# Kernel tuning notes

Measured on AMD Instinct MI355X. Metric: run time of the kernel, lower is better.

## Reference

```python
import jax, jax.numpy as jnp
import numpy as np

H = 64      # h_dim
E = 64      # embedding_dim
L = 100     # latent_dim
T = 30      # seq_len
DT = 0.03

def _leaky(x):
    return jnp.where(x >= 0, x, 0.01 * x)  # nn.LeakyReLU default slope

def _mlp(h, Ws, bs, Wf, bf):
    # 3 stacked [H,H] LeakyReLU layers + final [L,H] layer, LeakyReLU after EVERY layer (as in source)
    for i in range(Ws.shape[0]):
        h = _leaky(h @ Ws[i].T + bs[i])
    return _leaky(h @ Wf.T + bf)

def _lstm_step(h, c, gates):
    # torch LSTM gate order: i, f, g, o
    i, f, g, o = jnp.split(gates, 4, axis=-1)
    c = jax.nn.sigmoid(f) * c + jax.nn.sigmoid(i) * jnp.tanh(g)
    h = jax.nn.sigmoid(o) * jnp.tanh(c)
    return h, c

def _forward(expert_traj, init_state, eps,
             W_se, b_se,
             W_ih_e, W_hh_e, b_ih_e, b_hh_e,
             mean_Ws, mean_bs, mean_Wf, mean_bf,
             lv_Ws, lv_bs, lv_Wf, lv_bf,
             W_init, b_init,
             W_ih_d, W_hh_d, b_ih_d, b_hh_d,
             W_c, b_c):
    B = expert_traj.shape[0]
    # --- encode: relative positions ---
    rel_xy = jnp.concatenate([expert_traj[:, :1, :2],
                              expert_traj[:, 1:, :2] - expert_traj[:, :-1, :2]], axis=1)
    inp = jnp.concatenate([rel_xy, expert_traj[:, :, 2:]], axis=-1)  # [B,T,4]
    emb = inp @ W_se.T + b_se                                        # [B,T,E]
    x_seq = jnp.swapaxes(emb, 0, 1)                                  # [T,B,E] seq-major
    # precompute input projection for all timesteps in one GEMM
    xp = x_seq @ W_ih_e.T + (b_ih_e + b_hh_e)                        # [T,B,4H]
    h0 = jnp.zeros((B, H), dtype=expert_traj.dtype)
    c0 = jnp.zeros((B, H), dtype=expert_traj.dtype)
    def enc_step(carry, xp_t):
        h, c = carry
        h, c = _lstm_step(h, c, xp_t + h @ W_hh_e.T)
        return (h, c), None
    (hT, _), _ = jax.lax.scan(enc_step, (h0, c0), xp)
    mu = _mlp(hT, mean_Ws, mean_bs, mean_Wf, mean_bf)                # [B,L]
    log_var = _mlp(hT, lv_Ws, lv_bs, lv_Wf, lv_bf)                   # [B,L]
    # --- reparameterize + tanh ---
    z = jnp.tanh(eps * jnp.exp(0.5 * log_var) + mu)
    # --- decode ---
    dh = z @ W_init.T + b_init                                       # [B,H], h0 = c0 = dh
    bias_d = b_ih_d + b_hh_d
    def dec_step(carry, _):
        h, c, prev = carry
        xe = prev @ W_se.T + b_se                                    # spatial embedding of state
        h, c = _lstm_step(h, c, xe @ W_ih_d.T + h @ W_hh_d.T + bias_d)
        ctrl = h @ W_c.T + b_c                                       # [B,2]
        pedal = ctrl[:, 0]
        steer = jnp.clip(ctrl[:, 1], -0.5, 0.5)
        x_t, y_t, psi, v = prev[:, 0], prev[:, 1], prev[:, 2], prev[:, 3]
        v1 = jnp.clip(v + pedal * DT, 0.0, 30.0)
        psi_dot = jnp.clip(v * jnp.tan(steer) / 2.5, -3.14 / 2, 3.14 / 2)
        cur = jnp.stack([x_t + v * jnp.cos(psi) * DT,
                         y_t + v * jnp.sin(psi) * DT,
                         psi + psi_dot * DT,
                         v1], axis=1)
        return (h, c, cur), cur
    _, traj = jax.lax.scan(dec_step, (dh, dh, init_state), None, length=T)
    recons = jnp.swapaxes(traj, 0, 1)                                # [B,T,4]
    return recons, expert_traj, mu, log_var

def setup_inputs() -> dict:
    key = jax.random.key(0)
    ks = jax.random.split(key, 32)
    B = 16384
    s = 0.05
    def p(k, shape):
        return jax.random.normal(k, shape, dtype=jnp.float32) * s
    return {
        "expert_traj": jax.random.normal(ks[0], (B, T, 4), dtype=jnp.float32),
        "init_state": jax.random.normal(ks[1], (B, 4), dtype=jnp.float32),
        "eps": jax.random.normal(ks[2], (B, L), dtype=jnp.float32),
        "W_se": p(ks[3], (E, 4)), "b_se": p(ks[4], (E,)),
        "W_ih_e": p(ks[5], (4 * H, E)), "W_hh_e": p(ks[6], (4 * H, H)),
        "b_ih_e": p(ks[7], (4 * H,)), "b_hh_e": p(ks[8], (4 * H,)),
        "mean_Ws": p(ks[9], (3, H, H)), "mean_bs": p(ks[10], (3, H)),
        "mean_Wf": p(ks[11], (L, H)), "mean_bf": p(ks[12], (L,)),
        "lv_Ws": p(ks[13], (3, H, H)), "lv_bs": p(ks[14], (3, H)),
        "lv_Wf": p(ks[15], (L, H)), "lv_bf": p(ks[16], (L,)),
        "W_init": p(ks[17], (H, L)), "b_init": p(ks[18], (H,)),
        "W_ih_d": p(ks[19], (4 * H, E)), "W_hh_d": p(ks[20], (4 * H, H)),
        "b_ih_d": p(ks[21], (4 * H,)), "b_hh_d": p(ks[22], (4 * H,)),
        "W_c": p(ks[23], (2, H)), "b_c": p(ks[24], (2,)),
    }

def reference(expert_traj, init_state, eps,
              W_se, b_se,
              W_ih_e, W_hh_e, b_ih_e, b_hh_e,
              mean_Ws, mean_bs, mean_Wf, mean_bf,
              lv_Ws, lv_bs, lv_Wf, lv_bf,
              W_init, b_init,
              W_ih_d, W_hh_d, b_ih_d, b_hh_d,
              W_c, b_c):
    return _forward(expert_traj, init_state, eps,
                    W_se, b_se,
                    W_ih_e, W_hh_e, b_ih_e, b_hh_e,
                    mean_Ws, mean_bs, mean_Wf, mean_bf,
                    lv_Ws, lv_bs, lv_Wf, lv_bf,
                    W_init, b_init,
                    W_ih_d, W_hh_d, b_ih_d, b_hh_d,
                    W_c, b_c)
```

## Files before the change

### kernel.cpp

```cpp
#include <hip/hip_runtime.h>

typedef unsigned short u16;
typedef unsigned int u32;
typedef __attribute__((ext_vector_type(8))) short bf16x8;
typedef __attribute__((ext_vector_type(4))) float f32x4;

#define B_TOT 16384
#define RR 16
#define BLK 256
#define NBLK (B_TOT / RR)
#define TT 30
#define LL 100
#define DTC 0.03f
#define L2E 1.44269504088896f

#define HST 104
#define HBUF (RR * HST)

#define OFF_H   0
#define OFF_XS  6656
#define OFF_INP 10752
#define OFF_ZB  14592
#define SMEM_SZ 18944

#define WS_WHHE  0
#define WS_WHHD  18432
#define WS_MWS   36864
#define WS_LWS   49152
#define WS_MWF   61440
#define WS_LWF   67840
#define WS_WINIT 74240
#define WS_TOTAL 82432

__device__ __forceinline__ float bf2f(u16 u) {
    union { u32 i; float f; } v; v.i = ((u32)u) << 16; return v.f;
}
__device__ __forceinline__ u16 f2bf(float f) {
    union { float f; u32 i; } v; v.f = f;
    return (u16)((v.i + 0x7FFFu + ((v.i >> 16) & 1u)) >> 16);
}
__device__ __forceinline__ u16 f2bf_t(float f) {
    union { float f; u32 i; } v; v.f = f;
    return (u16)(v.i >> 16);
}
__device__ __forceinline__ float rcpf(float x) { return __builtin_amdgcn_rcpf(x); }
__device__ __forceinline__ float ex2(float x) { return __builtin_amdgcn_exp2f(x); }
__device__ __forceinline__ float tanh_(float x) {
    x = fminf(fmaxf(x, -15.f), 15.f);
    float e = __expf(2.f * x);
    return (e - 1.f) * rcpf(e + 1.f);
}
__device__ __forceinline__ float leaky(float x) { return x >= 0.f ? x : 0.01f * x; }
__device__ __forceinline__ f32x4 mfma16(bf16x8 a, bf16x8 b, f32x4 c) {
    return __builtin_amdgcn_mfma_f32_16x16x32_bf16(a, b, c, 0, 0, 0);
}

__global__ void setup_kernel(
    const float* __restrict__ W_se, const float* __restrict__ b_se,
    const float* __restrict__ W_ih_e, const float* __restrict__ W_hh_e,
    const float* __restrict__ b_ih_e, const float* __restrict__ b_hh_e,
    const float* __restrict__ W_ih_d, const float* __restrict__ W_hh_d,
    const float* __restrict__ b_ih_d, const float* __restrict__ b_hh_d,
    const float* __restrict__ mean_Ws, const float* __restrict__ lv_Ws,
    const float* __restrict__ mean_Wf, const float* __restrict__ lv_Wf,
    const float* __restrict__ W_init, u16* __restrict__ ws)
{
    const int gid = blockIdx.x * 256 + threadIdx.x;
    const int nth = gridDim.x * 256;
    for (int i = gid; i < 512; i += nth) {
        int which = i >> 8, row = i & 255, g = row >> 6;
        float s = (g == 2) ? 2.f * L2E : L2E;
        const float* wih = (which ? W_ih_d : W_ih_e) + row * 64;
        float f0=0,f1=0,f2=0,f3=0,fb=0;
        for (int e = 0; e < 64; ++e) {
            float w = wih[e];
            f0 = fmaf(w, W_se[e*4+0], f0);
            f1 = fmaf(w, W_se[e*4+1], f1);
            f2 = fmaf(w, W_se[e*4+2], f2);
            f3 = fmaf(w, W_se[e*4+3], f3);
            fb = fmaf(w, b_se[e], fb);
        }
        fb += (which ? b_ih_d : b_ih_e)[row] + (which ? b_hh_d : b_hh_e)[row];
        u16* dst = ws + (which ? WS_WHHD : WS_WHHE) + row * 72 + 64;
        dst[0]=f2bf(f0*s); dst[1]=f2bf(f1*s); dst[2]=f2bf(f2*s); dst[3]=f2bf(f3*s);
        dst[4]=f2bf(fb*s); dst[5]=0; dst[6]=0; dst[7]=0;
    }
    for (int i = gid; i < 2*16384; i += nth) {
        int which = i >= 16384;
        int j = which ? i - 16384 : i;
        int row = j >> 6, k = j & 63, g = row >> 6;
        float s = (g == 2) ? 2.f * L2E : L2E;
        const float* whh = which ? W_hh_d : W_hh_e;
        ws[(which ? WS_WHHD : WS_WHHE) + row*72 + k] = f2bf(whh[j] * s);
    }
    for (int i = gid; i < 12288; i += nth) {
        ws[WS_MWS + i] = f2bf(mean_Ws[i]);
        ws[WS_LWS + i] = f2bf(lv_Ws[i]);
    }
    for (int i = gid; i < 6400; i += nth) {
        ws[WS_MWF + i] = f2bf(mean_Wf[i]);
        ws[WS_LWF + i] = f2bf(lv_Wf[i]);
    }
    for (int i = gid; i < 8192; i += nth) {
        int r = i >> 7, k = i & 127;
        ws[WS_WINIT + i] = (k < LL) ? f2bf(W_init[r*LL + k]) : (u16)0;
    }
}

__global__ __launch_bounds__(BLK, 4) void vae_lstm_kernel(
    const float* __restrict__ expert, const float* __restrict__ init_state,
    const float* __restrict__ eps, const u16* __restrict__ ws,
    const float* __restrict__ mean_bs, const float* __restrict__ mean_bf,
    const float* __restrict__ lv_bs, const float* __restrict__ lv_bf,
    const float* __restrict__ b_init, const float* __restrict__ W_c,
    const float* __restrict__ b_c,
    float* __restrict__ out_recons, float* __restrict__ out_expert,
    float* __restrict__ out_mu, float* __restrict__ out_lv)
{
    const int tid = threadIdx.x;
    const int wv = tid >> 6;
    const int l = tid & 63;
    const int lcol = l & 15;
    const int quad = l >> 4;
    const int ubase = wv * 16;
    const int b0 = blockIdx.x * RR;

    __shared__ __align__(16) char smem[SMEM_SZ];
    u16* Hb  = (u16*)(smem + OFF_H);
    u16* XS  = (u16*)(smem + OFF_XS);
    u16* XA  = XS;
    u16* XB  = XS + RR*64;
    u16* inp = (u16*)(smem + OFF_INP);
    u16* zB  = (u16*)(smem + OFF_ZB);
    float* sc = (float*)XS;

    {
        u32* hz = (u32*)Hb;
        for (int idx = tid; idx < 2*RR*52; idx += BLK) hz[idx] = 0;
        u32* zz = (u32*)zB;
        for (int idx = tid; idx < RR*68; idx += BLK) zz[idx] = 0;
        __syncthreads();
        if (tid < 32) Hb[(tid >> 4)*HBUF + (tid & 15)*HST + 68] = 0x3F80;
        const int base = b0 * (TT*4);
        for (int idx = tid; idx < RR*TT*4; idx += BLK) {
            int row = idx / 120, q = idx % 120;
            int t = q >> 2, k = q & 3;
            float v = expert[base + idx];
            out_expert[base + idx] = v;
            float r = v;
            if (k < 2 && t > 0) r = v - expert[base + idx - 4];
            u16 hv = f2bf(r);
            inp[row*120 + q] = hv;
            if (t == 0) Hb[row*HST + 64 + k] = hv;
        }
        __syncthreads();
    }

    float cst[4] = {};
    float hval[4];
    bf16x8 bw[4][3];

    auto build_bw = [&](const u16* wsW) {
#pragma unroll
        for (int g = 0; g < 4; ++g) {
            const u16* wr = wsW + (g*64 + ubase + lcol) * 72;
            bw[g][0] = *(const bf16x8*)(wr + quad*8);
            bw[g][1] = *(const bf16x8*)(wr + 32 + quad*8);
            bw[g][2] = *(const bf16x8*)(wr + 64);
        }
#pragma unroll
        for (int g = 0; g < 4; ++g)
#pragma unroll
            for (int kk = 0; kk < 3; ++kk)
                asm volatile("" : "+v"(bw[g][kk]));
    };

    auto lstm_step = [&](const u16* Hc, u16* Hn) {
        const u16* hrow = Hc + lcol*HST;
        bf16x8 a0 = *(const bf16x8*)(hrow + quad*8);
        bf16x8 a1 = *(const bf16x8*)(hrow + 32 + quad*8);
        bf16x8 a2 = *(const bf16x8*)(hrow + 64 + quad*8);
        f32x4 acc[4];
#pragma unroll
        for (int g = 0; g < 4; ++g) {
            f32x4 z = {0.f, 0.f, 0.f, 0.f};
            z = mfma16(a0, bw[g][0], z);
            z = mfma16(a1, bw[g][1], z);
            acc[g] = mfma16(a2, bw[g][2], z);
        }
#pragma unroll
        for (int r = 0; r < 4; ++r) {
            float Ei = ex2(-acc[0][r]);
            float Ef = ex2(-acc[1][r]);
            float Eg = ex2(-acc[2][r]);
            float Eo = ex2(-acc[3][r]);
            float P = (1.f + Ei) * (1.f + Eg);
            float Q = 1.f + Ef;
            float num = fmaf(cst[r], P, (1.f - Eg) * Q);
            float cc = num * rcpf(P * Q);
            cst[r] = cc;
            float Ec = ex2(-2.f * L2E * cc);
            float h = (1.f - Ec) * rcpf((1.f + Eo) * (1.f + Ec));
            hval[r] = h;
            Hn[(quad*4 + r)*HST + ubase + lcol] = f2bf_t(h);
        }
    };

    build_bw(ws + WS_WHHE);
    for (int stp = 0; stp < TT; ++stp) {
        const u16* Hc = Hb + (stp & 1) * HBUF;
        u16* Hn = Hb + ((stp + 1) & 1) * HBUF;
        lstm_step(Hc, Hn);
        if (tid < 64 && stp < TT - 1) {
            int row = tid >> 2, k = tid & 3;
            Hn[row*HST + 64 + k] = inp[row*120 + (stp + 1)*4 + k];
        }
        __syncthreads();
    }
    u16* H0 = Hb;
    u16* H1 = Hb + HBUF;

    auto mlp_hidden = [&](const u16* inB, int ist, u16* outB, int ost,
                          const u16* wsW, const float* bg) {
        bf16x8 a0 = *(const bf16x8*)(inB + lcol*ist + quad*8);
        bf16x8 a1 = *(const bf16x8*)(inB + lcol*ist + 32 + quad*8);
        int n = ubase + lcol;
        const u16* wr = wsW + n*64;
        bf16x8 bb0 = *(const bf16x8*)(wr + quad*8);
        bf16x8 bb1 = *(const bf16x8*)(wr + 32 + quad*8);
        float bv = bg[n];
        f32x4 acc = {bv, bv, bv, bv};
        acc = mfma16(a0, bb0, acc);
        acc = mfma16(a1, bb1, acc);
#pragma unroll
        for (int r = 0; r < 4; ++r)
            outB[(quad*4 + r)*ost + n] = f2bf_t(leaky(acc[r]));
        __syncthreads();
    };

    mlp_hidden(H0, HST, XA, 64, ws + WS_MWS,        mean_bs);
    mlp_hidden(XA, 64,  XB, 64, ws + WS_MWS + 4096, mean_bs + 64);
    mlp_hidden(XB, 64,  XA, 64, ws + WS_MWS + 8192, mean_bs + 128);

    float muv[2][4];

    {
        bf16x8 fa = *(const bf16x8*)(XA + lcol*64 + quad*8);
        bf16x8 fb = *(const bf16x8*)(XA + lcol*64 + 32 + quad*8);
#pragma unroll
        for (int ti = 0; ti < 2; ++ti) {
            int nt = wv + ti*4;
            if (nt > 6) continue;
            int n = nt*16 + lcol;
            bool ok = (n < LL);
            bf16x8 bb0, bb1;
            if (ok) {
                const u16* wr = ws + WS_MWF + n*64;
                bb0 = *(const bf16x8*)(wr + quad*8);
                bb1 = *(const bf16x8*)(wr + 32 + quad*8);
            } else {
#pragma unroll
                for (int j = 0; j < 8; ++j) { bb0[j] = 0; bb1[j] = 0; }
            }
            float bv = ok ? mean_bf[n] : 0.f;
            f32x4 acc = {bv, bv, bv, bv};
            acc = mfma16(fa, bb0, acc);
            acc = mfma16(fb, bb1, acc);
#pragma unroll
            for (int r = 0; r < 4; ++r) {
                float vv = leaky(acc[r]);
                muv[ti][r] = vv;
                if (ok) out_mu[(size_t)(b0 + quad*4 + r) * LL + n] = vv;
            }
        }
    }

    mlp_hidden(H0, HST, H1, HST, ws + WS_LWS,        lv_bs);
    mlp_hidden(H1, HST, H0, HST, ws + WS_LWS + 4096, lv_bs + 64);
    mlp_hidden(H0, HST, H1, HST, ws + WS_LWS + 8192, lv_bs + 128);

    {
        bf16x8 fa = *(const bf16x8*)(H1 + lcol*HST + quad*8);
        bf16x8 fb = *(const bf16x8*)(H1 + lcol*HST + 32 + quad*8);
#pragma unroll
        for (int ti = 0; ti < 2; ++ti) {
            int nt = wv + ti*4;
            if (nt > 6) continue;
            int n = nt*16 + lcol;
            bool ok = (n < LL);
            bf16x8 bb0, bb1;
            if (ok) {
                const u16* wr = ws + WS_LWF + n*64;
                bb0 = *(const bf16x8*)(wr + quad*8);
                bb1 = *(const bf16x8*)(wr + 32 + quad*8);
            } else {
#pragma unroll
                for (int j = 0; j < 8; ++j) { bb0[j] = 0; bb1[j] = 0; }
            }
            float bv = ok ? lv_bf[n] : 0.f;
            f32x4 acc = {bv, bv, bv, bv};
            acc = mfma16(fa, bb0, acc);
            acc = mfma16(fb, bb1, acc);
#pragma unroll
            for (int r = 0; r < 4; ++r) {
                if (ok) {
                    float lv = leaky(acc[r]);
                    size_t gi = (size_t)(b0 + quad*4 + r) * LL + n;
                    out_lv[gi] = lv;
                    float zv = tanh_(fmaf(eps[gi], __expf(0.5f * lv), muv[ti][r]));
                    zB[(quad*4 + r)*136 + n] = f2bf_t(zv);
                }
            }
        }
        __syncthreads();
    }

    {
        bf16x8 az[4];
#pragma unroll
        for (int kt = 0; kt < 4; ++kt)
            az[kt] = *(const bf16x8*)(zB + lcol*136 + kt*32 + quad*8);
        int n = ubase + lcol;
        float bv = b_init[n];
        f32x4 acc = {bv, bv, bv, bv};
#pragma unroll
        for (int kt = 0; kt < 4; ++kt) {
            bf16x8 bi = *(const bf16x8*)(ws + WS_WINIT + n*128 + kt*32 + quad*8);
            acc = mfma16(az[kt], bi, acc);
        }
#pragma unroll
        for (int r = 0; r < 4; ++r) {
            cst[r] = acc[r];
            H0[(quad*4 + r)*HST + n] = f2bf_t(acc[r]);
        }
    }

    if (tid < 64) {
        int row = tid >> 2, k = tid & 3;
        H0[row*HST + 64 + k] = f2bf(init_state[(size_t)(b0 + row)*4 + k]);
    }
    float px = 0.f, py = 0.f, ppsi = 0.f, pv = 0.f;
    if (tid < 16) {
        const float* is = init_state + (size_t)(b0 + tid)*4;
        px = is[0]; py = is[1]; ppsi = is[2]; pv = is[3];
    }
    const float wc0 = W_c[ubase + lcol];
    const float wc1 = W_c[64 + ubase + lcol];
    const float bc0 = b_c[0], bc1 = b_c[1];
    build_bw(ws + WS_WHHD);
    __syncthreads();

    for (int stp = 0; stp < TT; ++stp) {
        const u16* Hc = Hb + (stp & 1) * HBUF;
        u16* Hn = Hb + ((stp + 1) & 1) * HBUF;
        lstm_step(Hc, Hn);
        float pa[4], pb[4];
#pragma unroll
        for (int r = 0; r < 4; ++r) {
            pa[r] = hval[r] * wc0;
            pb[r] = hval[r] * wc1;
        }
#pragma unroll
        for (int d = 1; d < 16; d <<= 1) {
#pragma unroll
            for (int r = 0; r < 4; ++r) {
                pa[r] += __shfl_xor(pa[r], d);
                pb[r] += __shfl_xor(pb[r], d);
            }
        }
        if (lcol == 0) {
#pragma unroll
            for (int r = 0; r < 4; ++r) {
                sc[wv*32 + quad*4 + r]      = pa[r];
                sc[wv*32 + 16 + quad*4 + r] = pb[r];
            }
        }
        __syncthreads();
        if (tid < 16) {
            int row = tid;
            float pedal = sc[row] + sc[32 + row] + sc[64 + row] + sc[96 + row] + bc0;
            float s1 = sc[16 + row] + sc[48 + row] + sc[80 + row] + sc[112 + row] + bc1;
            float steer = fminf(fmaxf(s1, -0.5f), 0.5f);
            float v1 = fminf(fmaxf(pv + pedal * DTC, 0.f), 30.f);
            float sn, cs;
            __sincosf(ppsi, &sn, &cs);
            float psid = fminf(fmaxf(pv * __tanf(steer) * 0.4f, -1.57f), 1.57f);
            float nx = fmaf(pv * cs, DTC, px);
            float ny = fmaf(pv * sn, DTC, py);
            float npsi = fmaf(psid, DTC, ppsi);
            px = nx; py = ny; ppsi = npsi; pv = v1;
            float4 o; o.x = nx; o.y = ny; o.z = npsi; o.w = v1;
            *(float4*)(out_recons + ((size_t)(b0 + row) * TT + stp) * 4) = o;
            u32 lo = (u32)f2bf(nx) | ((u32)f2bf(ny) << 16);
            u32 hi = (u32)f2bf(npsi) | ((u32)f2bf(v1) << 16);
            uint2 pk; pk.x = lo; pk.y = hi;
            *(uint2*)(Hn + row*HST + 64) = pk;
        }
        __syncthreads();
    }
}

extern "C" void kernel_launch(void* const* d_in, const int* in_sizes, int n_in,
                              void* d_out, int out_size, void* d_ws, size_t ws_size,
                              hipStream_t stream) {
    (void)in_sizes; (void)n_in; (void)ws_size; (void)out_size;
    const float* expert    = (const float*)d_in[0];
    const float* init_st   = (const float*)d_in[1];
    const float* eps       = (const float*)d_in[2];
    const float* W_se      = (const float*)d_in[3];
    const float* b_se      = (const float*)d_in[4];
    const float* W_ih_e    = (const float*)d_in[5];
    const float* W_hh_e    = (const float*)d_in[6];
    const float* b_ih_e    = (const float*)d_in[7];
    const float* b_hh_e    = (const float*)d_in[8];
    const float* mean_Ws   = (const float*)d_in[9];
    const float* mean_bs   = (const float*)d_in[10];
    const float* mean_Wf   = (const float*)d_in[11];
    const float* mean_bf   = (const float*)d_in[12];
    const float* lv_Ws     = (const float*)d_in[13];
    const float* lv_bs     = (const float*)d_in[14];
    const float* lv_Wf     = (const float*)d_in[15];
    const float* lv_bf     = (const float*)d_in[16];
    const float* W_init    = (const float*)d_in[17];
    const float* b_init    = (const float*)d_in[18];
    const float* W_ih_d    = (const float*)d_in[19];
    const float* W_hh_d    = (const float*)d_in[20];
    const float* b_ih_d    = (const float*)d_in[21];
    const float* b_hh_d    = (const float*)d_in[22];
    const float* W_c       = (const float*)d_in[23];
    const float* b_c       = (const float*)d_in[24];

    float* out = (float*)d_out;
    const size_t n_traj = (size_t)B_TOT * TT * 4;
    const size_t n_lat  = (size_t)B_TOT * LL;
    float* out_recons = out;
    float* out_expert = out + n_traj;
    float* out_mu     = out + 2 * n_traj;
    float* out_lv     = out + 2 * n_traj + n_lat;

    u16* ws = (u16*)d_ws;

    setup_kernel<<<64, 256, 0, stream>>>(
        W_se, b_se, W_ih_e, W_hh_e, b_ih_e, b_hh_e,
        W_ih_d, W_hh_d, b_ih_d, b_hh_d,
        mean_Ws, lv_Ws, mean_Wf, lv_Wf, W_init, ws);

    vae_lstm_kernel<<<NBLK, BLK, 0, stream>>>(
        expert, init_st, eps, ws,
        mean_bs, mean_bf, lv_bs, lv_bf, b_init, W_c, b_c,
        out_recons, out_expert, out_mu, out_lv);
}
```

Measured before the change: 233.6 us.

## Process 32 batch rows per block to reuse recurrent weight fragments

Doubles the rows per block from 16 to 32, so each wave runs two M-tiles of MFMA per LSTM step against the same register-resident W_hh fragments. This halves the block count and the per-row cost of weight loading and barriers. The MLP heads, decoder init and controller reduction are adjusted to cover both tiles. Shared memory doubles and launch bounds drop to 2 blocks per CU. The empty asm register pins on the weights are also removed. Fewer blocks may lower latency hiding in the serial recurrence.

```diff
diff --git a/kernel.cpp b/kernel.cpp
--- a/kernel.cpp
+++ b/kernel.cpp
@@ -6,7 +6,7 @@
 typedef __attribute__((ext_vector_type(4))) float f32x4;
 
 #define B_TOT 16384
-#define RR 16
+#define RR 32
 #define BLK 256
 #define NBLK (B_TOT / RR)
 #define TT 30
@@ -18,10 +18,10 @@
 #define HBUF (RR * HST)
 
 #define OFF_H   0
-#define OFF_XS  6656
-#define OFF_INP 10752
-#define OFF_ZB  14592
-#define SMEM_SZ 18944
+#define OFF_XS  13312
+#define OFF_INP 21504
+#define OFF_ZB  29184
+#define SMEM_SZ 37888
 
 #define WS_WHHE  0
 #define WS_WHHD  18432
@@ -107,7 +107,7 @@
     }
 }
 
-__global__ __launch_bounds__(BLK, 4) void vae_lstm_kernel(
+__global__ __launch_bounds__(BLK, 2) void vae_lstm_kernel(
     const float* __restrict__ expert, const float* __restrict__ init_state,
     const float* __restrict__ eps, const u16* __restrict__ ws,
     const float* __restrict__ mean_bs, const float* __restrict__ mean_bf,
@@ -136,13 +136,16 @@
 
     {
         u32* hz = (u32*)Hb;
-        for (int idx = tid; idx < 2*RR*52; idx += BLK) hz[idx] = 0;
+#pragma unroll
+        for (int i = 0; i < 13; ++i) hz[tid + i*BLK] = 0;
         u32* zz = (u32*)zB;
         for (int idx = tid; idx < RR*68; idx += BLK) zz[idx] = 0;
         __syncthreads();
-        if (tid < 32) Hb[(tid >> 4)*HBUF + (tid & 15)*HST + 68] = 0x3F80;
+        if (tid < 64) Hb[(tid >> 5)*HBUF + (tid & 31)*HST + 68] = 0x3F80;
         const int base = b0 * (TT*4);
-        for (int idx = tid; idx < RR*TT*4; idx += BLK) {
+#pragma unroll
+        for (int i = 0; i < 15; ++i) {
+            int idx = tid + i*BLK;
             int row = idx / 120, q = idx % 120;
             int t = q >> 2, k = q & 3;
             float v = expert[base + idx];
@@ -156,8 +159,8 @@
         __syncthreads();
     }
 
-    float cst[4] = {};
-    float hval[4];
+    float cst[2][4] = {};
+    float hval[2][4];
     bf16x8 bw[4][3];
 
     auto build_bw = [&](const u16* wsW) {
@@ -168,42 +171,45 @@
             bw[g][1] = *(const bf16x8*)(wr + 32 + quad*8);
             bw[g][2] = *(const bf16x8*)(wr + 64);
         }
-#pragma unroll
-        for (int g = 0; g < 4; ++g)
-#pragma unroll
-            for (int kk = 0; kk < 3; ++kk)
-                asm volatile("" : "+v"(bw[g][kk]));
     };
 
     auto lstm_step = [&](const u16* Hc, u16* Hn) {
-        const u16* hrow = Hc + lcol*HST;
-        bf16x8 a0 = *(const bf16x8*)(hrow + quad*8);
-        bf16x8 a1 = *(const bf16x8*)(hrow + 32 + quad*8);
-        bf16x8 a2 = *(const bf16x8*)(hrow + 64 + quad*8);
-        f32x4 acc[4];
-#pragma unroll
-        for (int g = 0; g < 4; ++g) {
-            f32x4 z = {0.f, 0.f, 0.f, 0.f};
-            z = mfma16(a0, bw[g][0], z);
-            z = mfma16(a1, bw[g][1], z);
-            acc[g] = mfma16(a2, bw[g][2], z);
-        }
-#pragma unroll
-        for (int r = 0; r < 4; ++r) {
-            float Ei = ex2(-acc[0][r]);
-            float Ef = ex2(-acc[1][r]);
-            float Eg = ex2(-acc[2][r]);
-            float Eo = ex2(-acc[3][r]);
-            float P = (1.f + Ei) * (1.f + Eg);
-            float Q = 1.f + Ef;
-            float num = fmaf(cst[r], P, (1.f - Eg) * Q);
-            float cc = num * rcpf(P * Q);
-            cst[r] = cc;
-            float Ec = ex2(-2.f * L2E * cc);
-            float h = (1.f - Ec) * rcpf((1.f + Eo) * (1.f + Ec));
-            hval[r] = h;
-            Hn[(quad*4 + r)*HST + ubase + lcol] = f2bf_t(h);
-        }
+        bf16x8 a0[2], a1[2], a2[2];
+#pragma unroll
+        for (int c = 0; c < 2; ++c) {
+            const u16* hrow = Hc + (c*16 + lcol)*HST;
+            a0[c] = *(const bf16x8*)(hrow + quad*8);
+            a1[c] = *(const bf16x8*)(hrow + 32 + quad*8);
+            a2[c] = *(const bf16x8*)(hrow + 64 + quad*8);
+        }
+        f32x4 acc[2][4];
+#pragma unroll
+        for (int c = 0; c < 2; ++c)
+#pragma unroll
+            for (int g = 0; g < 4; ++g) {
+                f32x4 z = {0.f, 0.f, 0.f, 0.f};
+                z = mfma16(a0[c], bw[g][0], z);
+                z = mfma16(a1[c], bw[g][1], z);
+                acc[c][g] = mfma16(a2[c], bw[g][2], z);
+            }
+#pragma unroll
+        for (int c = 0; c < 2; ++c)
+#pragma unroll
+            for (int r = 0; r < 4; ++r) {
+                float Ei = ex2(-acc[c][0][r]);
+                float Ef = ex2(-acc[c][1][r]);
+                float Eg = ex2(-acc[c][2][r]);
+                float Eo = ex2(-acc[c][3][r]);
+                float P = (1.f + Ei) * (1.f + Eg);
+                float Q = 1.f + Ef;
+                float num = fmaf(cst[c][r], P, (1.f - Eg) * Q);
+                float cc = num * rcpf(P * Q);
+                cst[c][r] = cc;
+                float Ec = ex2(-2.f * L2E * cc);
+                float h = (1.f - Ec) * rcpf((1.f + Eo) * (1.f + Ec));
+                hval[c][r] = h;
+                Hn[(c*16 + quad*4 + r)*HST + ubase + lcol] = f2bf_t(h);
+            }
     };
 
     build_bw(ws + WS_WHHE);
@@ -211,7 +217,7 @@
         const u16* Hc = Hb + (stp & 1) * HBUF;
         u16* Hn = Hb + ((stp + 1) & 1) * HBUF;
         lstm_step(Hc, Hn);
-        if (tid < 64 && stp < TT - 1) {
+        if (tid < 128 && stp < TT - 1) {
             int row = tid >> 2, k = tid & 3;
             Hn[row*HST + 64 + k] = inp[row*120 + (stp + 1)*4 + k];
         }
@@ -222,19 +228,22 @@
 
     auto mlp_hidden = [&](const u16* inB, int ist, u16* outB, int ost,
                           const u16* wsW, const float* bg) {
-        bf16x8 a0 = *(const bf16x8*)(inB + lcol*ist + quad*8);
-        bf16x8 a1 = *(const bf16x8*)(inB + lcol*ist + 32 + quad*8);
         int n = ubase + lcol;
         const u16* wr = wsW + n*64;
         bf16x8 bb0 = *(const bf16x8*)(wr + quad*8);
         bf16x8 bb1 = *(const bf16x8*)(wr + 32 + quad*8);
         float bv = bg[n];
-        f32x4 acc = {bv, bv, bv, bv};
-        acc = mfma16(a0, bb0, acc);
-        acc = mfma16(a1, bb1, acc);
-#pragma unroll
-        for (int r = 0; r < 4; ++r)
-            outB[(quad*4 + r)*ost + n] = f2bf_t(leaky(acc[r]));
+#pragma unroll
+        for (int c = 0; c < 2; ++c) {
+            bf16x8 a0 = *(const bf16x8*)(inB + (c*16 + lcol)*ist + quad*8);
+            bf16x8 a1 = *(const bf16x8*)(inB + (c*16 + lcol)*ist + 32 + quad*8);
+            f32x4 acc = {bv, bv, bv, bv};
+            acc = mfma16(a0, bb0, acc);
+            acc = mfma16(a1, bb1, acc);
+#pragma unroll
+            for (int r = 0; r < 4; ++r)
+                outB[(c*16 + quad*4 + r)*ost + n] = f2bf_t(leaky(acc[r]));
+        }
         __syncthreads();
     };
 
@@ -242,15 +251,14 @@
     mlp_hidden(XA, 64,  XB, 64, ws + WS_MWS + 4096, mean_bs + 64);
     mlp_hidden(XB, 64,  XA, 64, ws + WS_MWS + 8192, mean_bs + 128);
 
-    float muv[2][4];
+    float muv[4][4];
 
     {
-        bf16x8 fa = *(const bf16x8*)(XA + lcol*64 + quad*8);
-        bf16x8 fb = *(const bf16x8*)(XA + lcol*64 + 32 + quad*8);
-#pragma unroll
-        for (int ti = 0; ti < 2; ++ti) {
-            int nt = wv + ti*4;
-            if (nt > 6) continue;
+#pragma unroll
+        for (int ti = 0; ti < 4; ++ti) {
+            int t = wv + ti*4;
+            if (t >= 14) continue;
+            int nt = t >> 1, Mtl = t & 1;
             int n = nt*16 + lcol;
             bool ok = (n < LL);
             bf16x8 bb0, bb1;
@@ -263,6 +271,8 @@
                 for (int j = 0; j < 8; ++j) { bb0[j] = 0; bb1[j] = 0; }
             }
             float bv = ok ? mean_bf[n] : 0.f;
+            bf16x8 fa = *(const bf16x8*)(XA + (Mtl*16 + lcol)*64 + quad*8);
+            bf16x8 fb = *(const bf16x8*)(XA + (Mtl*16 + lcol)*64 + 32 + quad*8);
             f32x4 acc = {bv, bv, bv, bv};
             acc = mfma16(fa, bb0, acc);
             acc = mfma16(fb, bb1, acc);
@@ -270,7 +280,7 @@
             for (int r = 0; r < 4; ++r) {
                 float vv = leaky(acc[r]);
                 muv[ti][r] = vv;
-                if (ok) out_mu[(size_t)(b0 + quad*4 + r) * LL + n] = vv;
+                if (ok) out_mu[(size_t)(b0 + Mtl*16 + quad*4 + r) * LL + n] = vv;
             }
         }
     }
@@ -280,12 +290,11 @@
     mlp_hidden(H0, HST, H1, HST, ws + WS_LWS + 8192, lv_bs + 128);
 
     {
-        bf16x8 fa = *(const bf16x8*)(H1 + lcol*HST + quad*8);
-        bf16x8 fb = *(const bf16x8*)(H1 + lcol*HST + 32 + quad*8);
-#pragma unroll
-        for (int ti = 0; ti < 2; ++ti) {
-            int nt = wv + ti*4;
-            if (nt > 6) continue;
+#pragma unroll
+        for (int ti = 0; ti < 4; ++ti) {
+            int t = wv + ti*4;
+            if (t >= 14) continue;
+            int nt = t >> 1, Mtl = t & 1;
             int n = nt*16 + lcol;
             bool ok = (n < LL);
             bf16x8 bb0, bb1;
@@ -298,6 +307,8 @@
                 for (int j = 0; j < 8; ++j) { bb0[j] = 0; bb1[j] = 0; }
             }
             float bv = ok ? lv_bf[n] : 0.f;
+            bf16x8 fa = *(const bf16x8*)(H1 + (Mtl*16 + lcol)*HST + quad*8);
+            bf16x8 fb = *(const bf16x8*)(H1 + (Mtl*16 + lcol)*HST + 32 + quad*8);
             f32x4 acc = {bv, bv, bv, bv};
             acc = mfma16(fa, bb0, acc);
             acc = mfma16(fb, bb1, acc);
@@ -305,10 +316,10 @@
             for (int r = 0; r < 4; ++r) {
                 if (ok) {
                     float lv = leaky(acc[r]);
-                    size_t gi = (size_t)(b0 + quad*4 + r) * LL + n;
+                    size_t gi = (size_t)(b0 + Mtl*16 + quad*4 + r) * LL + n;
                     out_lv[gi] = lv;
                     float zv = tanh_(fmaf(eps[gi], __expf(0.5f * lv), muv[ti][r]));
-                    zB[(quad*4 + r)*136 + n] = f2bf_t(zv);
+                    zB[(Mtl*16 + quad*4 + r)*136 + n] = f2bf_t(zv);
                 }
             }
         }
@@ -316,31 +327,31 @@
     }
 
     {
-        bf16x8 az[4];
-#pragma unroll
-        for (int kt = 0; kt < 4; ++kt)
-            az[kt] = *(const bf16x8*)(zB + lcol*136 + kt*32 + quad*8);
         int n = ubase + lcol;
         float bv = b_init[n];
-        f32x4 acc = {bv, bv, bv, bv};
-#pragma unroll
-        for (int kt = 0; kt < 4; ++kt) {
-            bf16x8 bi = *(const bf16x8*)(ws + WS_WINIT + n*128 + kt*32 + quad*8);
-            acc = mfma16(az[kt], bi, acc);
-        }
-#pragma unroll
-        for (int r = 0; r < 4; ++r) {
-            cst[r] = acc[r];
-            H0[(quad*4 + r)*HST + n] = f2bf_t(acc[r]);
-        }
-    }
-
-    if (tid < 64) {
+#pragma unroll
+        for (int c = 0; c < 2; ++c) {
+            f32x4 acc = {bv, bv, bv, bv};
+#pragma unroll
+            for (int kt = 0; kt < 4; ++kt) {
+                bf16x8 az = *(const bf16x8*)(zB + (c*16 + lcol)*136 + kt*32 + quad*8);
+                bf16x8 bi = *(const bf16x8*)(ws + WS_WINIT + n*128 + kt*32 + quad*8);
+                acc = mfma16(az, bi, acc);
+            }
+#pragma unroll
+            for (int r = 0; r < 4; ++r) {
+                cst[c][r] = acc[r];
+                H0[(c*16 + quad*4 + r)*HST + n] = f2bf_t(acc[r]);
+            }
+        }
+    }
+
+    if (tid < 128) {
         int row = tid >> 2, k = tid & 3;
         H0[row*HST + 64 + k] = f2bf(init_state[(size_t)(b0 + row)*4 + k]);
     }
     float px = 0.f, py = 0.f, ppsi = 0.f, pv = 0.f;
-    if (tid < 16) {
+    if (tid < 32) {
         const float* is = init_state + (size_t)(b0 + tid)*4;
         px = is[0]; py = is[1]; ppsi = is[2]; pv = is[3];
     }
@@ -354,32 +365,39 @@
         const u16* Hc = Hb + (stp & 1) * HBUF;
         u16* Hn = Hb + ((stp + 1) & 1) * HBUF;
         lstm_step(Hc, Hn);
-        float pa[4], pb[4];
-#pragma unroll
-        for (int r = 0; r < 4; ++r) {
-            pa[r] = hval[r] * wc0;
-            pb[r] = hval[r] * wc1;
-        }
+        float pa[2][4], pb[2][4];
+#pragma unroll
+        for (int c = 0; c < 2; ++c)
+#pragma unroll
+            for (int r = 0; r < 4; ++r) {
+                pa[c][r] = hval[c][r] * wc0;
+                pb[c][r] = hval[c][r] * wc1;
+            }
 #pragma unroll
         for (int d = 1; d < 16; d <<= 1) {
 #pragma unroll
-            for (int r = 0; r < 4; ++r) {
-                pa[r] += __shfl_xor(pa[r], d);
-                pb[r] += __shfl_xor(pb[r], d);
-            }
+            for (int c = 0; c < 2; ++c)
+#pragma unroll
+                for (int r = 0; r < 4; ++r) {
+                    pa[c][r] += __shfl_xor(pa[c][r], d);
+                    pb[c][r] += __shfl_xor(pb[c][r], d);
+                }
         }
         if (lcol == 0) {
 #pragma unroll
-            for (int r = 0; r < 4; ++r) {
-                sc[wv*32 + quad*4 + r]      = pa[r];
-                sc[wv*32 + 16 + quad*4 + r] = pb[r];
-            }
-        }
-        __syncthreads();
-        if (tid < 16) {
-            int row = tid;
-            float pedal = sc[row] + sc[32 + row] + sc[64 + row] + sc[96 + row] + bc0;
-            float s1 = sc[16 + row] + sc[48 + row] + sc[80 + row] + sc[112 + row] + bc1;
+            for (int c = 0; c < 2; ++c)
+#pragma unroll
+                for (int r = 0; r < 4; ++r) {
+                    sc[c*128 + wv*32 + quad*4 + r]      = pa[c][r];
+                    sc[c*128 + wv*32 + 16 + quad*4 + r] = pb[c][r];
+                }
+        }
+        __syncthreads();
+        if (tid < 32) {
+            int row = tid, c = tid >> 4, rl = tid & 15;
+            const float* s = sc + c*128;
+            float pedal = s[rl] + s[32 + rl] + s[64 + rl] + s[96 + rl] + bc0;
+            float s1 = s[16 + rl] + s[48 + rl] + s[80 + rl] + s[112 + rl] + bc1;
             float steer = fminf(fmaxf(s1, -0.5f), 0.5f);
             float v1 = fminf(fmaxf(pv + pedal * DTC, 0.f), 30.f);
             float sn, cs;
```

New measurement: 243.6 us. 1.04x slower.

## Process 32 batch rows per 512-thread block with two M-tiles of waves

Applied to the files above, without the earlier changes.

The block now covers 32 batch rows with 8 waves instead of 16 rows with 4 waves. Waves are split into two M-tiles that each handle 16 rows, and the shared-memory layout is reorganised. The mu values are now staged in shared memory instead of registers so both MLP heads can use one shared routine, and the preprocessing stages the raw trajectory in LDS. This halves the block count and spreads the MLP tail over more waves, but each barrier now synchronises 8 waves, LDS use per block grows, and the asm pinning of the weight fragments to registers is removed.

```diff
diff --git a/kernel.cpp b/kernel.cpp
--- a/kernel.cpp
+++ b/kernel.cpp
@@ -6,8 +6,8 @@
 typedef __attribute__((ext_vector_type(4))) float f32x4;
 
 #define B_TOT 16384
-#define RR 16
-#define BLK 256
+#define RR 32
+#define BLK 512
 #define NBLK (B_TOT / RR)
 #define TT 30
 #define LL 100
@@ -15,13 +15,13 @@
 #define L2E 1.44269504088896f
 
 #define HST 104
-#define HBUF (RR * HST)
+#define HBUF_U16 (RR * HST)
 
 #define OFF_H   0
-#define OFF_XS  6656
-#define OFF_INP 10752
-#define OFF_ZB  14592
-#define SMEM_SZ 18944
+#define OFF_XB  13312
+#define OFF_Z   22528
+#define OFF_U   31232
+#define SMEM_SZ 38912
 
 #define WS_WHHE  0
 #define WS_WHHD  18432
@@ -118,65 +118,68 @@
     float* __restrict__ out_mu, float* __restrict__ out_lv)
 {
     const int tid = threadIdx.x;
+    const int b0g = blockIdx.x * RR;
     const int wv = tid >> 6;
-    const int l = tid & 63;
-    const int lcol = l & 15;
-    const int quad = l >> 4;
-    const int ubase = wv * 16;
-    const int b0 = blockIdx.x * RR;
+    const int Mt = wv >> 2;
+    const int wsub = wv & 3;
+    const int lane = tid & 63;
+    const int lcol = lane & 15;
+    const int quad = lane >> 4;
+    const int jcol = wsub * 16 + lcol;
 
     __shared__ __align__(16) char smem[SMEM_SZ];
-    u16* Hb  = (u16*)(smem + OFF_H);
-    u16* XS  = (u16*)(smem + OFF_XS);
-    u16* XA  = XS;
-    u16* XB  = XS + RR*64;
-    u16* inp = (u16*)(smem + OFF_INP);
-    u16* zB  = (u16*)(smem + OFF_ZB);
-    float* sc = (float*)XS;
+    u16* Hbuf  = (u16*)(smem + OFF_H);
+    u16* XB0   = (u16*)(smem + OFF_XB);
+    u16* XB1   = XB0 + RR * 72;
+    u16* zBuf  = (u16*)(smem + OFF_Z);
+    u16* inp   = (u16*)(smem + OFF_U);
+    u16* muB   = (u16*)(smem + OFF_U);
+    float* sRaw  = (float*)(smem + OFF_XB);
+    float* sc    = (float*)(smem + OFF_XB);
 
     {
-        u32* hz = (u32*)Hb;
-        for (int idx = tid; idx < 2*RR*52; idx += BLK) hz[idx] = 0;
-        u32* zz = (u32*)zB;
-        for (int idx = tid; idx < RR*68; idx += BLK) zz[idx] = 0;
-        __syncthreads();
-        if (tid < 32) Hb[(tid >> 4)*HBUF + (tid & 15)*HST + 68] = 0x3F80;
-        const int base = b0 * (TT*4);
+        const int base = b0g * (TT*4);
+        u32* hz = (u32*)Hbuf;
+        for (int idx = tid; idx < HBUF_U16; idx += BLK) hz[idx] = 0;
         for (int idx = tid; idx < RR*TT*4; idx += BLK) {
-            int row = idx / 120, q = idx % 120;
-            int t = q >> 2, k = q & 3;
             float v = expert[base + idx];
+            sRaw[idx] = v;
             out_expert[base + idx] = v;
-            float r = v;
-            if (k < 2 && t > 0) r = v - expert[base + idx - 4];
-            u16 hv = f2bf(r);
-            inp[row*120 + q] = hv;
-            if (t == 0) Hb[row*HST + 64 + k] = hv;
-        }
-        __syncthreads();
-    }
-
-    float cst[4] = {};
+        }
+        __syncthreads();
+        for (int idx = tid; idx < RR*TT*4; idx += BLK) {
+            int q = idx % (TT*4);
+            int k = q & 3, t = q >> 2;
+            int row = idx / (TT*4);
+            float v = sRaw[idx];
+            if (k < 2 && t > 0) v -= sRaw[idx - 4];
+            u16 hv = f2bf(v);
+            inp[idx] = hv;
+            if (t == 0) Hbuf[row*HST + 64 + k] = hv;
+            if (q == 0) {
+                Hbuf[row*HST + 68] = 0x3F80;
+                Hbuf[HBUF_U16 + row*HST + 68] = 0x3F80;
+            }
+        }
+        __syncthreads();
+    }
+
+    float creg[4] = {0.f, 0.f, 0.f, 0.f};
     float hval[4];
     bf16x8 bw[4][3];
 
     auto build_bw = [&](const u16* wsW) {
 #pragma unroll
         for (int g = 0; g < 4; ++g) {
-            const u16* wr = wsW + (g*64 + ubase + lcol) * 72;
+            const u16* wr = wsW + (g*64 + jcol) * 72;
             bw[g][0] = *(const bf16x8*)(wr + quad*8);
             bw[g][1] = *(const bf16x8*)(wr + 32 + quad*8);
             bw[g][2] = *(const bf16x8*)(wr + 64);
         }
-#pragma unroll
-        for (int g = 0; g < 4; ++g)
-#pragma unroll
-            for (int kk = 0; kk < 3; ++kk)
-                asm volatile("" : "+v"(bw[g][kk]));
     };
 
     auto lstm_step = [&](const u16* Hc, u16* Hn) {
-        const u16* hrow = Hc + lcol*HST;
+        const u16* hrow = Hc + (Mt*16 + lcol)*HST;
         bf16x8 a0 = *(const bf16x8*)(hrow + quad*8);
         bf16x8 a1 = *(const bf16x8*)(hrow + 32 + quad*8);
         bf16x8 a2 = *(const bf16x8*)(hrow + 64 + quad*8);
@@ -196,163 +199,139 @@
             float Eo = ex2(-acc[3][r]);
             float P = (1.f + Ei) * (1.f + Eg);
             float Q = 1.f + Ef;
-            float num = fmaf(cst[r], P, (1.f - Eg) * Q);
+            float num = fmaf(creg[r], P, (1.f - Eg) * Q);
             float cc = num * rcpf(P * Q);
-            cst[r] = cc;
+            creg[r] = cc;
             float Ec = ex2(-2.f * L2E * cc);
             float h = (1.f - Ec) * rcpf((1.f + Eo) * (1.f + Ec));
             hval[r] = h;
-            Hn[(quad*4 + r)*HST + ubase + lcol] = f2bf_t(h);
+            Hn[(Mt*16 + quad*4 + r)*HST + jcol] = f2bf_t(h);
         }
     };
 
     build_bw(ws + WS_WHHE);
     for (int stp = 0; stp < TT; ++stp) {
-        const u16* Hc = Hb + (stp & 1) * HBUF;
-        u16* Hn = Hb + ((stp + 1) & 1) * HBUF;
+        const u16* Hc = Hbuf + (stp & 1) * HBUF_U16;
+        u16* Hn = Hbuf + ((stp + 1) & 1) * HBUF_U16;
         lstm_step(Hc, Hn);
-        if (tid < 64 && stp < TT - 1) {
+        if (tid < 128 && stp < TT-1) {
             int row = tid >> 2, k = tid & 3;
-            Hn[row*HST + 64 + k] = inp[row*120 + (stp + 1)*4 + k];
-        }
-        __syncthreads();
-    }
-    u16* H0 = Hb;
-    u16* H1 = Hb + HBUF;
-
-    auto mlp_hidden = [&](const u16* inB, int ist, u16* outB, int ost,
+            Hn[row*HST + 64 + k] = inp[row*(TT*4) + (stp+1)*4 + k];
+        }
+        __syncthreads();
+    }
+
+    {
+        u32* zb = (u32*)zBuf;
+        for (int idx = tid; idx < RR*136/2; idx += BLK) zb[idx] = 0;
+    }
+
+    auto mlp_hidden = [&](const u16* inB, int inStride, u16* outB,
                           const u16* wsW, const float* bg) {
-        bf16x8 a0 = *(const bf16x8*)(inB + lcol*ist + quad*8);
-        bf16x8 a1 = *(const bf16x8*)(inB + lcol*ist + 32 + quad*8);
-        int n = ubase + lcol;
-        const u16* wr = wsW + n*64;
+        float bv = bg[jcol];
+        const u16* wr = wsW + jcol*64;
         bf16x8 bb0 = *(const bf16x8*)(wr + quad*8);
         bf16x8 bb1 = *(const bf16x8*)(wr + 32 + quad*8);
-        float bv = bg[n];
         f32x4 acc = {bv, bv, bv, bv};
+        bf16x8 a0 = *(const bf16x8*)(inB + (Mt*16 + lcol)*inStride + quad*8);
+        bf16x8 a1 = *(const bf16x8*)(inB + (Mt*16 + lcol)*inStride + 32 + quad*8);
         acc = mfma16(a0, bb0, acc);
         acc = mfma16(a1, bb1, acc);
 #pragma unroll
         for (int r = 0; r < 4; ++r)
-            outB[(quad*4 + r)*ost + n] = f2bf_t(leaky(acc[r]));
+            outB[(Mt*16 + quad*4 + r)*72 + jcol] = f2bf_t(leaky(acc[r]));
         __syncthreads();
     };
 
-    mlp_hidden(H0, HST, XA, 64, ws + WS_MWS,        mean_bs);
-    mlp_hidden(XA, 64,  XB, 64, ws + WS_MWS + 4096, mean_bs + 64);
-    mlp_hidden(XB, 64,  XA, 64, ws + WS_MWS + 8192, mean_bs + 128);
-
-    float muv[2][4];
-
-    {
-        bf16x8 fa = *(const bf16x8*)(XA + lcol*64 + quad*8);
-        bf16x8 fb = *(const bf16x8*)(XA + lcol*64 + 32 + quad*8);
+    auto mlp_final = [&](const u16* inB, const u16* wsW, const float* bg, int mode) {
 #pragma unroll
         for (int ti = 0; ti < 2; ++ti) {
-            int nt = wv + ti*4;
-            if (nt > 6) continue;
+            int t = wv + ti*8;
+            if (t >= 14) continue;
+            int nt = t >> 1, Mtl = t & 1;
             int n = nt*16 + lcol;
             bool ok = (n < LL);
+            float bv = ok ? bg[n] : 0.f;
             bf16x8 bb0, bb1;
             if (ok) {
-                const u16* wr = ws + WS_MWF + n*64;
+                const u16* wr = wsW + n*64;
                 bb0 = *(const bf16x8*)(wr + quad*8);
                 bb1 = *(const bf16x8*)(wr + 32 + quad*8);
             } else {
 #pragma unroll
                 for (int j = 0; j < 8; ++j) { bb0[j] = 0; bb1[j] = 0; }
             }
-            float bv = ok ? mean_bf[n] : 0.f;
             f32x4 acc = {bv, bv, bv, bv};
-            acc = mfma16(fa, bb0, acc);
-            acc = mfma16(fb, bb1, acc);
-#pragma unroll
-            for (int r = 0; r < 4; ++r) {
-                float vv = leaky(acc[r]);
-                muv[ti][r] = vv;
-                if (ok) out_mu[(size_t)(b0 + quad*4 + r) * LL + n] = vv;
-            }
-        }
-    }
-
-    mlp_hidden(H0, HST, H1, HST, ws + WS_LWS,        lv_bs);
-    mlp_hidden(H1, HST, H0, HST, ws + WS_LWS + 4096, lv_bs + 64);
-    mlp_hidden(H0, HST, H1, HST, ws + WS_LWS + 8192, lv_bs + 128);
-
-    {
-        bf16x8 fa = *(const bf16x8*)(H1 + lcol*HST + quad*8);
-        bf16x8 fb = *(const bf16x8*)(H1 + lcol*HST + 32 + quad*8);
-#pragma unroll
-        for (int ti = 0; ti < 2; ++ti) {
-            int nt = wv + ti*4;
-            if (nt > 6) continue;
-            int n = nt*16 + lcol;
-            bool ok = (n < LL);
-            bf16x8 bb0, bb1;
+            bf16x8 a0 = *(const bf16x8*)(inB + (Mtl*16 + lcol)*72 + quad*8);
+            bf16x8 a1 = *(const bf16x8*)(inB + (Mtl*16 + lcol)*72 + 32 + quad*8);
+            acc = mfma16(a0, bb0, acc);
+            acc = mfma16(a1, bb1, acc);
             if (ok) {
-                const u16* wr = ws + WS_LWF + n*64;
-                bb0 = *(const bf16x8*)(wr + quad*8);
-                bb1 = *(const bf16x8*)(wr + 32 + quad*8);
-            } else {
-#pragma unroll
-                for (int j = 0; j < 8; ++j) { bb0[j] = 0; bb1[j] = 0; }
-            }
-            float bv = ok ? lv_bf[n] : 0.f;
-            f32x4 acc = {bv, bv, bv, bv};
-            acc = mfma16(fa, bb0, acc);
-            acc = mfma16(fb, bb1, acc);
-#pragma unroll
-            for (int r = 0; r < 4; ++r) {
-                if (ok) {
-                    float lv = leaky(acc[r]);
-                    size_t gi = (size_t)(b0 + quad*4 + r) * LL + n;
-                    out_lv[gi] = lv;
-                    float zv = tanh_(fmaf(eps[gi], __expf(0.5f * lv), muv[ti][r]));
-                    zB[(quad*4 + r)*136 + n] = f2bf_t(zv);
+#pragma unroll
+                for (int r = 0; r < 4; ++r) {
+                    int m = Mtl*16 + quad*4 + r;
+                    float vv = leaky(acc[r]);
+                    size_t gi = (size_t)(b0g + m) * LL + n;
+                    if (mode == 0) {
+                        muB[m*LL + n] = f2bf_t(vv);
+                        out_mu[gi] = vv;
+                    } else {
+                        out_lv[gi] = vv;
+                        float mu = bf2f(muB[m*LL + n]);
+                        float zv = tanh_(fmaf(eps[gi], __expf(0.5f * vv), mu));
+                        zBuf[m*136 + n] = f2bf_t(zv);
+                    }
                 }
             }
         }
         __syncthreads();
-    }
+    };
+
+    mlp_hidden(Hbuf, HST, XB0, ws + WS_MWS, mean_bs);
+    mlp_hidden(XB0, 72, XB1, ws + WS_MWS + 4096, mean_bs + 64);
+    mlp_hidden(XB1, 72, XB0, ws + WS_MWS + 8192, mean_bs + 128);
+    mlp_final(XB0, ws + WS_MWF, mean_bf, 0);
+    mlp_hidden(Hbuf, HST, XB0, ws + WS_LWS, lv_bs);
+    mlp_hidden(XB0, 72, XB1, ws + WS_LWS + 4096, lv_bs + 64);
+    mlp_hidden(XB1, 72, XB0, ws + WS_LWS + 8192, lv_bs + 128);
+    mlp_final(XB0, ws + WS_LWF, lv_bf, 1);
 
     {
-        bf16x8 az[4];
-#pragma unroll
-        for (int kt = 0; kt < 4; ++kt)
-            az[kt] = *(const bf16x8*)(zB + lcol*136 + kt*32 + quad*8);
-        int n = ubase + lcol;
-        float bv = b_init[n];
+        float bv = b_init[jcol];
+        const u16* wr = ws + WS_WINIT + jcol*128;
         f32x4 acc = {bv, bv, bv, bv};
 #pragma unroll
         for (int kt = 0; kt < 4; ++kt) {
-            bf16x8 bi = *(const bf16x8*)(ws + WS_WINIT + n*128 + kt*32 + quad*8);
-            acc = mfma16(az[kt], bi, acc);
+            bf16x8 az = *(const bf16x8*)(zBuf + (Mt*16 + lcol)*136 + kt*32 + quad*8);
+            bf16x8 bi = *(const bf16x8*)(wr + kt*32 + quad*8);
+            acc = mfma16(az, bi, acc);
         }
 #pragma unroll
         for (int r = 0; r < 4; ++r) {
-            cst[r] = acc[r];
-            H0[(quad*4 + r)*HST + n] = f2bf_t(acc[r]);
-        }
-    }
-
-    if (tid < 64) {
-        int row = tid >> 2, k = tid & 3;
-        H0[row*HST + 64 + k] = f2bf(init_state[(size_t)(b0 + row)*4 + k]);
-    }
+            creg[r] = acc[r];
+            Hbuf[(Mt*16 + quad*4 + r)*HST + jcol] = f2bf_t(acc[r]);
+        }
+        __syncthreads();
+        if (tid < RR*4) {
+            int row = tid >> 2, k = tid & 3;
+            Hbuf[row*HST + 64 + k] = f2bf(init_state[b0g*4 + tid]);
+        }
+        __syncthreads();
+    }
+
     float px = 0.f, py = 0.f, ppsi = 0.f, pv = 0.f;
-    if (tid < 16) {
-        const float* is = init_state + (size_t)(b0 + tid)*4;
+    if (tid < 32) {
+        const float* is = init_state + (size_t)(b0g + tid)*4;
         px = is[0]; py = is[1]; ppsi = is[2]; pv = is[3];
     }
-    const float wc0 = W_c[ubase + lcol];
-    const float wc1 = W_c[64 + ubase + lcol];
+    const float wc0 = W_c[jcol];
+    const float wc1 = W_c[64 + jcol];
     const float bc0 = b_c[0], bc1 = b_c[1];
     build_bw(ws + WS_WHHD);
-    __syncthreads();
 
     for (int stp = 0; stp < TT; ++stp) {
-        const u16* Hc = Hb + (stp & 1) * HBUF;
-        u16* Hn = Hb + ((stp + 1) & 1) * HBUF;
+        const u16* Hc = Hbuf + (stp & 1) * HBUF_U16;
+        u16* Hn = Hbuf + ((stp + 1) & 1) * HBUF_U16;
         lstm_step(Hc, Hn);
         float pa[4], pb[4];
 #pragma unroll
@@ -371,15 +350,16 @@
         if (lcol == 0) {
 #pragma unroll
             for (int r = 0; r < 4; ++r) {
-                sc[wv*32 + quad*4 + r]      = pa[r];
-                sc[wv*32 + 16 + quad*4 + r] = pb[r];
+                sc[Mt*128 + wsub*32 + quad*4 + r]      = pa[r];
+                sc[Mt*128 + wsub*32 + 16 + quad*4 + r] = pb[r];
             }
         }
         __syncthreads();
-        if (tid < 16) {
-            int row = tid;
-            float pedal = sc[row] + sc[32 + row] + sc[64 + row] + sc[96 + row] + bc0;
-            float s1 = sc[16 + row] + sc[48 + row] + sc[80 + row] + sc[112 + row] + bc1;
+        if (tid < 32) {
+            int row = tid, Mt2 = tid >> 4, ri = tid & 15;
+            const float* s = sc + Mt2*128;
+            float pedal = s[ri] + s[32 + ri] + s[64 + ri] + s[96 + ri] + bc0;
+            float s1 = s[16 + ri] + s[48 + ri] + s[80 + ri] + s[112 + ri] + bc1;
             float steer = fminf(fmaxf(s1, -0.5f), 0.5f);
             float v1 = fminf(fmaxf(pv + pedal * DTC, 0.f), 30.f);
             float sn, cs;
@@ -390,7 +370,7 @@
             float npsi = fmaf(psid, DTC, ppsi);
             px = nx; py = ny; ppsi = npsi; pv = v1;
             float4 o; o.x = nx; o.y = ny; o.z = npsi; o.w = v1;
-            *(float4*)(out_recons + ((size_t)(b0 + row) * TT + stp) * 4) = o;
+            *(float4*)(out_recons + ((size_t)(b0g + row) * TT + stp) * 4) = o;
             u32 lo = (u32)f2bf(nx) | ((u32)f2bf(ny) << 16);
             u32 hi = (u32)f2bf(npsi) | ((u32)f2bf(v1) << 16);
             uint2 pk; pk.x = lo; pk.y = hi;
```

Result: no change. 235.2 us (+0.7%).
